# Kernel tuning notes

Hardware: AMD Instinct MI355X
Metric: run time of the kernel (lower is better)

Reference implementation:

```python
import jax, jax.numpy as jnp
import numpy as np

B, N, E = 32, 2048, 4096
D_IN, C, H = 256, 64, 4          # node_hidden_size, gnn_hidden_size, num_heads
SLOPE = 0.2                       # PyG GATConv default negative_slope


def gat_conv(x, src, dst, W, att_src, att_dst, bias):
    """One PyG-style GATConv (concat=True, add_self_loops=True) on a single graph.
    x: [N, Din]; src/dst: [E] int; W: [Din, H*C]; att_*: [H, C]; bias: [H*C]."""
    n = x.shape[0]
    h = (x @ W).reshape(n, H, C)                       # [N,H,C]
    a_src = jnp.einsum('nhc,hc->nh', h, att_src)       # [N,H]
    a_dst = jnp.einsum('nhc,hc->nh', h, att_dst)
    loop = jnp.arange(n, dtype=src.dtype)              # self loops
    s = jnp.concatenate([src, loop])
    d = jnp.concatenate([dst, loop])
    e = jax.nn.leaky_relu(a_src[s] + a_dst[d], SLOPE)  # [E+N,H]
    # segment softmax over incoming edges of each target node
    m = jax.ops.segment_max(e, d, num_segments=n)
    ex = jnp.exp(e - m[d])
    denom = jax.ops.segment_sum(ex, d, num_segments=n)
    alpha = ex / (denom[d] + 1e-16)                    # [E+N,H]
    out = jax.ops.segment_sum(alpha[:, :, None] * h[s], d, num_segments=n)  # [N,H,C]
    return out.reshape(n, H * C) + bias


def setup_inputs() -> dict:
    key = jax.random.key(0)
    ks = jax.random.split(key, 12)
    g = lambda k, shp, fan: jax.random.normal(k, shp, jnp.float32) * (1.0 / np.sqrt(fan))
    return {
        'node_embeddings': jax.random.normal(ks[0], (B, N, D_IN), jnp.float32),
        'src_index': jax.random.randint(ks[1], (B, E), 0, N, jnp.int32),
        'tgt_index': jax.random.randint(ks[2], (B, E), 0, N, jnp.int32),
        'W1': g(ks[3], (D_IN, H * C), D_IN),
        'att_src1': g(ks[4], (H, C), C),
        'att_dst1': g(ks[5], (H, C), C),
        'bias1': jnp.zeros((H * C,), jnp.float32),
        'W2': g(ks[6], (H * C, H * C), H * C),
        'att_src2': g(ks[7], (H, C), C),
        'att_dst2': g(ks[8], (H, C), C),
        'bias2': jnp.zeros((H * C,), jnp.float32),
    }


def reference(node_embeddings, src_index, tgt_index, W1, att_src1, att_dst1, bias1,
              W2, att_src2, att_dst2, bias2):
    def per_graph(x, s, d):
        m = gat_conv(x, s, d, W1, att_src1, att_dst1, bias1)
        m = jax.nn.elu(m)                              # dropout = identity (eval)
        m = gat_conv(m, s, d, W2, att_src2, att_dst2, bias2)
        return m
    return jax.vmap(per_graph)(node_embeddings, src_index, tgt_index)  # [B,N,H*C]
```

## Files before the change

### kernel.cpp

```cpp
#include <hip/hip_runtime.h>
#include <hip/hip_bf16.h>
#include <cstdint>

#define BB 32
#define NN 2048
#define EE 4096
#define HH 4
#define CC 64
#define DD 256
#define MM (BB*NN)

typedef __attribute__((ext_vector_type(8))) short bf16x8;
typedef __attribute__((ext_vector_type(8))) unsigned short u16x8;
typedef __attribute__((ext_vector_type(4))) float f32x4;

__device__ __forceinline__ float b2f(__hip_bfloat16 x){ return __bfloat162float(x); }
__device__ __forceinline__ float u2f(unsigned short u){ return __uint_as_float((unsigned)u << 16); }
__device__ __forceinline__ unsigned short f2u(float f){
  __hip_bfloat16 h = __float2bfloat16(f);
  return *(unsigned short*)&h;
}
__device__ __forceinline__ float ldany(const void* p, int isf, size_t i){
  return isf ? ((const float*)p)[i] : b2f(((const __hip_bfloat16*)p)[i]);
}
__device__ __forceinline__ void gld_lds16(const void* g, void* l){
  __builtin_amdgcn_global_load_lds((const __attribute__((address_space(1))) uint32_t*)g,
                                   (__attribute__((address_space(3))) uint32_t*)l, 16, 0, 0);
}

__global__ void detect_kernel(const unsigned* __restrict__ w, int* __restrict__ flag){
  __shared__ int cnt;
  if(threadIdx.x == 0) cnt = 0;
  __syncthreads();
  int c = 0;
  #pragma unroll
  for(int i = 0; i < 4; ++i){
    unsigned v = w[threadIdx.x*4 + i];
    unsigned elo = (v >> 7) & 0xFFu;
    if(elo >= 100u && elo <= 150u) ++c;
  }
  atomicAdd(&cnt, c);
  __syncthreads();
  if(threadIdx.x == 0) *flag = (cnt < 128) ? 1 : 0;
}

__global__ __launch_bounds__(256) void prep_kernel(const void* __restrict__ W1,
    const void* __restrict__ W2, __hip_bfloat16* __restrict__ W1t,
    __hip_bfloat16* __restrict__ W2t,
    const void* s0, const void* s1, const void* s2, const void* s3,
    const void* s4, const void* s5, float* __restrict__ attf,
    int* __restrict__ degc, const int* __restrict__ flag)
{
  int isf = *flag;
  int bid = blockIdx.x, t = threadIdx.x;
  if(bid < 512){
    const void* W = (bid < 256) ? W1 : W2;
    __hip_bfloat16* WT = (bid < 256) ? W1t : W2t;
    int i = (bid & 255)*256 + t;
    WT[i] = __float2bfloat16(ldany(W, isf, (size_t)(i & 255)*256 + (i >> 8)));
  } else if(bid < 518){
    int i = (bid - 512)*256 + t;
    int seg = i >> 8, off = i & 255;
    const void* s = seg==0?s0 : seg==1?s1 : seg==2?s2 : seg==3?s3 : seg==4?s4 : s5;
    attf[i] = ldany(s, isf, off);
  } else {
    int i = (bid - 518)*256 + t;
    int4 z = {0,0,0,0};
    *((int4*)degc + i) = z;
  }
}

template<int DYNA>
__global__ __launch_bounds__(256) void mfma_gemm(const void* __restrict__ Ap,
    const __hip_bfloat16* __restrict__ BT, __hip_bfloat16* __restrict__ C,
    const float* __restrict__ attS, const float* __restrict__ attD,
    float* __restrict__ aS, float* __restrict__ aD, const int* __restrict__ flag)
{
  __shared__ __align__(16) short lds[128*128];
  short* lA = lds;
  short* lB = lds + 128*64;
  const int isf  = DYNA ? *flag : 0;
  const int tid  = threadIdx.x;
  const int w    = tid >> 6, lane = tid & 63;
  const int dd   = blockIdx.x;
  const int xcd  = dd & 7, slot = dd >> 3;
  const int rb   = xcd*64 + (slot >> 1), cb = slot & 1;
  const int row0 = rb*128, col0 = cb*128;
  const int wr   = (w & 1)*64, wc = (w >> 1)*64;
  const int lr   = lane >> 3;
  const int kb_g = (lane & 7) ^ lr;
  const int fm   = lane & 15, quad = lane >> 4;
  f32x4 acc[4][4] = {};

  for(int k0 = 0; k0 < 256; k0 += 64){
    #pragma unroll
    for(int c = 0; c < 4; ++c){
      int ra = w*32 + c*8;
      const short* gb = (const short*)BT + (size_t)(col0 + ra + lr)*DD + k0 + kb_g*8;
      gld_lds16(gb, &lB[ra*64]);
    }
    if(DYNA && isf){
      const float* Af = (const float*)Ap;
      float4 ta[4], tb[4];
      #pragma unroll
      for(int i = 0; i < 4; ++i){
        int f8 = i*256 + tid;
        int m = f8 >> 3, kb = f8 & 7;
        const float* p = Af + (size_t)(row0 + m)*DD + k0 + kb*8;
        ta[i] = *(const float4*)p;
        tb[i] = *(const float4*)(p + 4);
      }
      #pragma unroll
      for(int i = 0; i < 4; ++i){
        int f8 = i*256 + tid;
        int m = f8 >> 3, kb = f8 & 7;
        u16x8 o;
        o[0] = f2u(ta[i].x); o[1] = f2u(ta[i].y); o[2] = f2u(ta[i].z); o[3] = f2u(ta[i].w);
        o[4] = f2u(tb[i].x); o[5] = f2u(tb[i].y); o[6] = f2u(tb[i].z); o[7] = f2u(tb[i].w);
        *(u16x8*)&lA[m*64 + ((kb ^ (m & 7))*8)] = o;
      }
    } else {
      #pragma unroll
      for(int c = 0; c < 4; ++c){
        int ra = w*32 + c*8;
        const short* ga = (const short*)Ap + (size_t)(row0 + ra + lr)*DD + k0 + kb_g*8;
        gld_lds16(ga, &lA[ra*64]);
      }
    }
    __syncthreads();
    #pragma unroll
    for(int ks = 0; ks < 2; ++ks){
      bf16x8 af[4], bfr[4];
      int kb = ks*4 + quad;
      #pragma unroll
      for(int i = 0; i < 4; ++i){
        int m = wr + i*16 + fm;
        af[i]  = *(const bf16x8*)&lA[m*64 + ((kb ^ (m & 7))*8)];
        int n = wc + i*16 + fm;
        bfr[i] = *(const bf16x8*)&lB[n*64 + ((kb ^ (n & 7))*8)];
      }
      #pragma unroll
      for(int i = 0; i < 4; ++i)
        #pragma unroll
        for(int j = 0; j < 4; ++j)
          acc[i][j] = __builtin_amdgcn_mfma_f32_16x16x32_bf16(af[i], bfr[j], acc[i][j], 0, 0, 0);
    }
    __syncthreads();
  }

  const int headI = (col0 + wc) >> 6;
  float ws_[4], wd_[4];
  #pragma unroll
  for(int j = 0; j < 4; ++j){
    ws_[j] = attS[headI*CC + j*16 + fm];
    wd_[j] = attD[headI*CC + j*16 + fm];
  }
  #pragma unroll
  for(int i = 0; i < 4; ++i){
    #pragma unroll
    for(int r = 0; r < 4; ++r){
      float s = 0.f, dv = 0.f;
      #pragma unroll
      for(int j = 0; j < 4; ++j){
        float v = acc[i][j][r];
        s  += v * ws_[j];
        dv += v * wd_[j];
      }
      #pragma unroll
      for(int m = 1; m <= 8; m <<= 1){
        s  += __shfl_xor(s,  m);
        dv += __shfl_xor(dv, m);
      }
      if(fm == i*4 + r){
        int row = row0 + wr + i*16 + quad*4 + r;
        aS[(size_t)row*HH + headI] = s;
        aD[(size_t)row*HH + headI] = dv;
      }
    }
  }

  #pragma unroll
  for(int i = 0; i < 4; ++i)
    #pragma unroll
    for(int j = 0; j < 4; ++j)
      #pragma unroll
      for(int r = 0; r < 4; ++r){
        int rl = wr + i*16 + quad*4 + r;
        int cl = wc + j*16 + fm;
        lds[rl*128 + (cl ^ ((rl & 12) << 2))] = (short)f2u(acc[i][j][r]);
      }
  __syncthreads();
  const int rr = tid >> 4, cc = (tid & 15)*8;
  #pragma unroll
  for(int p = 0; p < 8; ++p){
    int rl = p*16 + rr;
    u16x8 v = *(const u16x8*)&lds[rl*128 + (cc ^ ((rl & 12) << 2))];
    *(u16x8*)((unsigned short*)C + (size_t)(row0 + rl)*DD + col0 + cc) = v;
  }
}

__global__ __launch_bounds__(256) void deg_kernel(const int* __restrict__ dst, int* __restrict__ degc)
{
  int idx = blockIdx.x*256 + threadIdx.x;
  if(idx >= BB*EE) return;
  int b = idx >> 12;
  atomicAdd(&degc[b*NN + dst[idx]], 1);
}

__global__ __launch_bounds__(256) void scan_kernel(int* __restrict__ degc, int* __restrict__ row_ptr)
{
  __shared__ int part[256];
  int b = blockIdx.x, t = threadIdx.x;
  int loc[8], s = 0;
  #pragma unroll
  for(int i = 0; i < 8; ++i){ loc[i] = s; s += degc[b*NN + t*8 + i]; }
  part[t] = s;
  __syncthreads();
  if(t == 0){
    int run = 0;
    for(int i = 0; i < 256; ++i){ int tmp = part[i]; part[i] = run; run += tmp; }
  }
  __syncthreads();
  int base = b*EE + part[t];
  #pragma unroll
  for(int i = 0; i < 8; ++i){
    int v = base + loc[i];
    row_ptr[b*(NN+1) + t*8 + i] = v;
    degc   [b*NN     + t*8 + i] = v;
  }
  if(t == 255) row_ptr[b*(NN+1) + NN] = base + s;
}

__global__ __launch_bounds__(256) void scatter_kernel(const int* __restrict__ src,
    const int* __restrict__ dst, int* __restrict__ cursor, unsigned short* __restrict__ srcList)
{
  int idx = blockIdx.x*256 + threadIdx.x;
  if(idx >= BB*EE) return;
  int b = idx >> 12;
  int pos = atomicAdd(&cursor[b*NN + dst[idx]], 1);
  srcList[pos] = (unsigned short)src[idx];
}

template<int LAYER>
__global__ __launch_bounds__(256) void gather_kernel(const __hip_bfloat16* __restrict__ H,
    const float* __restrict__ a_src, const float* __restrict__ a_dst,
    const int* __restrict__ row_ptr, const unsigned short* __restrict__ srcList,
    const float* __restrict__ bias, void* __restrict__ outp,
    const int* __restrict__ flag)
{
  int blk  = blockIdx.x;
  int vblk = (blk & 7)*2048 + (blk >> 3);
  int wid  = vblk*4 + (int)(threadIdx.x >> 6);
  int lane = threadIdx.x & 63;
  int b = wid >> 11, d = wid & (NN-1);
  int head = lane >> 4;
  int start = row_ptr[b*(NN+1) + d];
  int end   = row_ptr[b*(NN+1) + d + 1];
  const unsigned short* Hu = (const unsigned short*)H;

  float adv = a_dst[wid*HH + head];
  float sv  = a_src[wid*HH + head] + adv;
  sv = sv > 0.f ? sv : 0.2f*sv;
  float exs = __expf(sv);

  ushort4 hv = *(const ushort4*)(Hu + (size_t)wid*DD + lane*4);
  f32x4 acc;
  acc.x = exs*u2f(hv.x); acc.y = exs*u2f(hv.y); acc.z = exs*u2f(hv.z); acc.w = exs*u2f(hv.w);
  float den = exs;

  int e = start;
  int s = 0; float ax = 0.f;
  if(e < end){ s = srcList[e]; ax = a_src[(b*NN + s)*HH + head]; }
  while(e < end){
    int sn = 0; float axn = 0.f;
    if(e + 1 < end){ sn = srcList[e+1]; axn = a_src[(b*NN + sn)*HH + head]; }
    float v = ax + adv;
    v = v > 0.f ? v : 0.2f*v;
    float ex = __expf(v);
    ushort4 hw = *(const ushort4*)(Hu + (size_t)(b*NN + s)*DD + lane*4);
    acc.x += ex*u2f(hw.x); acc.y += ex*u2f(hw.y); acc.z += ex*u2f(hw.z); acc.w += ex*u2f(hw.w);
    den += ex;
    s = sn; ax = axn; ++e;
  }
  float inv = 1.f / (den + 1e-16f);
  float4 bs = *(const float4*)(bias + lane*4);
  float o0 = acc.x*inv + bs.x, o1 = acc.y*inv + bs.y;
  float o2 = acc.z*inv + bs.z, o3 = acc.w*inv + bs.w;
  size_t oi = (size_t)wid*DD + lane*4;
  if(LAYER == 1){
    o0 = o0 > 0.f ? o0 : expm1f(o0);
    o1 = o1 > 0.f ? o1 : expm1f(o1);
    o2 = o2 > 0.f ? o2 : expm1f(o2);
    o3 = o3 > 0.f ? o3 : expm1f(o3);
    ushort4 ov = { f2u(o0), f2u(o1), f2u(o2), f2u(o3) };
    *(ushort4*)((unsigned short*)outp + oi) = ov;
  } else {
    if(*flag){
      float4 ov = { o0, o1, o2, o3 };
      *(float4*)((float*)outp + oi) = ov;
    } else {
      ushort4 ov = { f2u(o0), f2u(o1), f2u(o2), f2u(o3) };
      *(ushort4*)((unsigned short*)outp + oi) = ov;
    }
  }
}

extern "C" void kernel_launch(void* const* d_in, const int* in_sizes, int n_in,
                              void* d_out, int out_size, void* d_ws, size_t ws_size,
                              hipStream_t stream)
{
  const void* x_in = d_in[0];
  const int*  srcI = (const int*)d_in[1];
  const int*  dstI = (const int*)d_in[2];
  const void* W1   = d_in[3];
  const void* as1  = d_in[4];
  const void* ad1  = d_in[5];
  const void* b1   = d_in[6];
  const void* W2   = d_in[7];
  const void* as2  = d_in[8];
  const void* ad2  = d_in[9];
  const void* b2   = d_in[10];

  char* ws = (char*)d_ws;
  __hip_bfloat16* R1  = (__hip_bfloat16*)ws; ws += (size_t)MM*DD*2;
  __hip_bfloat16* R2  = (__hip_bfloat16*)ws; ws += (size_t)MM*DD*2;
  float* a_src = (float*)ws; ws += (size_t)MM*HH*4;
  float* a_dst = (float*)ws; ws += (size_t)MM*HH*4;
  __hip_bfloat16* W1t = (__hip_bfloat16*)ws; ws += (size_t)DD*DD*2;
  __hip_bfloat16* W2t = (__hip_bfloat16*)ws; ws += (size_t)DD*DD*2;
  float* attf = (float*)ws; ws += 1536*4;
  int*   degc = (int*)ws;   ws += (size_t)BB*NN*4;
  int*   rowp = (int*)ws;   ws += (size_t)BB*(NN+1)*4;
  unsigned short* srcL = (unsigned short*)ws; ws += (size_t)BB*EE*2;
  int*   flag = (int*)ws;   ws += 8;

  const int gemmBlocks   = (MM/128)*(DD/128);
  const int edgeBlocks   = (BB*EE)/256;
  const int gatherBlocks = (MM*64)/256;

  detect_kernel<<<1, 64, 0, stream>>>((const unsigned*)x_in, flag);
  prep_kernel<<<582, 256, 0, stream>>>(W1, W2, W1t, W2t,
                                       as1, ad1, b1, as2, ad2, b2, attf, degc, flag);

  deg_kernel    <<<edgeBlocks, 256, 0, stream>>>(dstI, degc);
  scan_kernel   <<<BB,         256, 0, stream>>>(degc, rowp);
  scatter_kernel<<<edgeBlocks, 256, 0, stream>>>(srcI, dstI, degc, srcL);

  mfma_gemm<1><<<gemmBlocks, 256, 0, stream>>>(x_in, W1t, R2, attf + 0, attf + 256,
                                               a_src, a_dst, flag);
  gather_kernel<1><<<gatherBlocks, 256, 0, stream>>>(R2, a_src, a_dst, rowp, srcL,
                                                     attf + 512, R1, flag);
  mfma_gemm<0><<<gemmBlocks, 256, 0, stream>>>(R1, W2t, R2, attf + 768, attf + 1024,
                                               a_src, a_dst, flag);
  gather_kernel<2><<<gatherBlocks, 256, 0, stream>>>(R2, a_src, a_dst, rowp, srcL,
                                                     attf + 1280, d_out, flag);
}
```

Baseline: 242.6 us.

## Double-buffer GEMM LDS tiles with K=32 stages and prefetch neighbor rows in aggregation

The GEMM main loop is split into eight K=32 stages. It ping-pongs two LDS buffers so the global-to-LDS loads for the next stage are issued before the MFMAs on the current stage, which needs only one barrier per stage. For fp32 input, the next A tile is held in registers and written to LDS after the compute. The launch bounds now request 4 blocks per CU, and the LDS swizzle is redone for 32-wide rows. In the edge aggregation kernel, the neighbor feature row is now prefetched one edge ahead along with the attention score, hiding gather latency at the cost of more registers.

```diff
diff --git a/kernel.cpp b/kernel.cpp
--- a/kernel.cpp
+++ b/kernel.cpp
@@ -71,14 +71,12 @@
 }
 
 template<int DYNA>
-__global__ __launch_bounds__(256) void mfma_gemm(const void* __restrict__ Ap,
+__global__ __launch_bounds__(256, 4) void mfma_gemm(const void* __restrict__ Ap,
     const __hip_bfloat16* __restrict__ BT, __hip_bfloat16* __restrict__ C,
     const float* __restrict__ attS, const float* __restrict__ attD,
     float* __restrict__ aS, float* __restrict__ aD, const int* __restrict__ flag)
 {
-  __shared__ __align__(16) short lds[128*128];
-  short* lA = lds;
-  short* lB = lds + 128*64;
+  __shared__ __align__(16) short lds[16384];
   const int isf  = DYNA ? *flag : 0;
   const int tid  = threadIdx.x;
   const int w    = tid >> 6, lane = tid & 63;
@@ -87,64 +85,86 @@
   const int rb   = xcd*64 + (slot >> 1), cb = slot & 1;
   const int row0 = rb*128, col0 = cb*128;
   const int wr   = (w & 1)*64, wc = (w >> 1)*64;
-  const int lr   = lane >> 3;
-  const int kb_g = (lane & 7) ^ lr;
   const int fm   = lane & 15, quad = lane >> 4;
+  const int srow = lane >> 2;
+  const int sslot= lane & 3;
   f32x4 acc[4][4] = {};
 
-  for(int k0 = 0; k0 < 256; k0 += 64){
+  const float* Af = (const float*)Ap;
+  const short* Ab = (const short*)Ap;
+  const int fr = tid >> 1;
+  const int fh = tid & 1;
+  float4 fa0, fa1, fa2, fa3;
+
+  auto stageB = [&](int t, int cur){
+    short* lB = lds + cur*8192 + 4096;
     #pragma unroll
-    for(int c = 0; c < 4; ++c){
-      int ra = w*32 + c*8;
-      const short* gb = (const short*)BT + (size_t)(col0 + ra + lr)*DD + k0 + kb_g*8;
-      gld_lds16(gb, &lB[ra*64]);
-    }
-    if(DYNA && isf){
-      const float* Af = (const float*)Ap;
-      float4 ta[4], tb[4];
-      #pragma unroll
-      for(int i = 0; i < 4; ++i){
-        int f8 = i*256 + tid;
-        int m = f8 >> 3, kb = f8 & 7;
-        const float* p = Af + (size_t)(row0 + m)*DD + k0 + kb*8;
-        ta[i] = *(const float4*)p;
-        tb[i] = *(const float4*)(p + 4);
-      }
-      #pragma unroll
-      for(int i = 0; i < 4; ++i){
-        int f8 = i*256 + tid;
-        int m = f8 >> 3, kb = f8 & 7;
-        u16x8 o;
-        o[0] = f2u(ta[i].x); o[1] = f2u(ta[i].y); o[2] = f2u(ta[i].z); o[3] = f2u(ta[i].w);
-        o[4] = f2u(tb[i].x); o[5] = f2u(tb[i].y); o[6] = f2u(tb[i].z); o[7] = f2u(tb[i].w);
-        *(u16x8*)&lA[m*64 + ((kb ^ (m & 7))*8)] = o;
-      }
-    } else {
-      #pragma unroll
-      for(int c = 0; c < 4; ++c){
-        int ra = w*32 + c*8;
-        const short* ga = (const short*)Ap + (size_t)(row0 + ra + lr)*DD + k0 + kb_g*8;
-        gld_lds16(ga, &lA[ra*64]);
-      }
-    }
-    __syncthreads();
+    for(int c = 0; c < 2; ++c){
+      int rB = w*32 + c*16 + srow;
+      const short* gb = (const short*)BT + (size_t)(col0 + rB)*DD + t*32
+                        + ((sslot ^ ((rB ^ (rB >> 3)) & 3))*8);
+      gld_lds16(gb, lB + (w*32 + c*16)*32);
+    }
+  };
+  auto stageA16 = [&](int t, int cur){
+    short* lA = lds + cur*8192;
     #pragma unroll
-    for(int ks = 0; ks < 2; ++ks){
-      bf16x8 af[4], bfr[4];
-      int kb = ks*4 + quad;
+    for(int c = 0; c < 2; ++c){
+      int rA = w*32 + c*16 + srow;
+      const short* ga = Ab + (size_t)(row0 + rA)*DD + t*32
+                        + ((sslot ^ ((rA ^ (rA >> 3)) & 3))*8);
+      gld_lds16(ga, lA + (w*32 + c*16)*32);
+    }
+  };
+  auto loadA32 = [&](int t){
+    const float* p = Af + (size_t)(row0 + fr)*DD + t*32 + fh*16;
+    fa0 = ((const float4*)p)[0]; fa1 = ((const float4*)p)[1];
+    fa2 = ((const float4*)p)[2]; fa3 = ((const float4*)p)[3];
+  };
+  auto writeA32 = [&](int cur){
+    short* lA = lds + cur*8192;
+    int sg = (fr ^ (fr >> 3)) & 3;
+    u16x8 o0, o1;
+    o0[0]=f2u(fa0.x); o0[1]=f2u(fa0.y); o0[2]=f2u(fa0.z); o0[3]=f2u(fa0.w);
+    o0[4]=f2u(fa1.x); o0[5]=f2u(fa1.y); o0[6]=f2u(fa1.z); o0[7]=f2u(fa1.w);
+    o1[0]=f2u(fa2.x); o1[1]=f2u(fa2.y); o1[2]=f2u(fa2.z); o1[3]=f2u(fa2.w);
+    o1[4]=f2u(fa3.x); o1[5]=f2u(fa3.y); o1[6]=f2u(fa3.z); o1[7]=f2u(fa3.w);
+    *(u16x8*)(lA + fr*32 + (((2*fh  ) ^ sg)*8)) = o0;
+    *(u16x8*)(lA + fr*32 + (((2*fh+1) ^ sg)*8)) = o1;
+  };
+
+  if(DYNA && isf){ loadA32(0); writeA32(0); }
+  else           { stageA16(0, 0); }
+  stageB(0, 0);
+  __syncthreads();
+
+  #pragma unroll 2
+  for(int t = 0; t < 8; ++t){
+    const int cur = t & 1, nxt = cur ^ 1;
+    const bool pre = (t < 7);
+    if(pre){
+      if(DYNA && isf) loadA32(t+1);
+      else            stageA16(t+1, nxt);
+      stageB(t+1, nxt);
+    }
+    {
+      const short* lA = lds + cur*8192;
+      const short* lB = lds + cur*8192 + 4096;
+      bf16x8 af[4], bfv[4];
       #pragma unroll
       for(int i = 0; i < 4; ++i){
         int m = wr + i*16 + fm;
-        af[i]  = *(const bf16x8*)&lA[m*64 + ((kb ^ (m & 7))*8)];
+        af[i]  = *(const bf16x8*)&lA[m*32 + ((quad ^ ((m ^ (m >> 3)) & 3))*8)];
         int n = wc + i*16 + fm;
-        bfr[i] = *(const bf16x8*)&lB[n*64 + ((kb ^ (n & 7))*8)];
+        bfv[i] = *(const bf16x8*)&lB[n*32 + ((quad ^ ((n ^ (n >> 3)) & 3))*8)];
       }
       #pragma unroll
       for(int i = 0; i < 4; ++i)
         #pragma unroll
         for(int j = 0; j < 4; ++j)
-          acc[i][j] = __builtin_amdgcn_mfma_f32_16x16x32_bf16(af[i], bfr[j], acc[i][j], 0, 0, 0);
-    }
+          acc[i][j] = __builtin_amdgcn_mfma_f32_16x16x32_bf16(af[i], bfv[j], acc[i][j], 0, 0, 0);
+    }
+    if(pre && DYNA && isf) writeA32(nxt);
     __syncthreads();
   }
 
@@ -269,18 +289,25 @@
   float den = exs;
 
   int e = start;
-  int s = 0; float ax = 0.f;
-  if(e < end){ s = srcList[e]; ax = a_src[(b*NN + s)*HH + head]; }
+  float ax = 0.f; ushort4 hw = {0,0,0,0};
+  if(e < end){
+    int s = srcList[e];
+    ax = a_src[(b*NN + s)*HH + head];
+    hw = *(const ushort4*)(Hu + (size_t)(b*NN + s)*DD + lane*4);
+  }
   while(e < end){
-    int sn = 0; float axn = 0.f;
-    if(e + 1 < end){ sn = srcList[e+1]; axn = a_src[(b*NN + sn)*HH + head]; }
+    float axn = 0.f; ushort4 hwn = {0,0,0,0};
+    if(e + 1 < end){
+      int sn = srcList[e+1];
+      axn = a_src[(b*NN + sn)*HH + head];
+      hwn = *(const ushort4*)(Hu + (size_t)(b*NN + sn)*DD + lane*4);
+    }
     float v = ax + adv;
     v = v > 0.f ? v : 0.2f*v;
     float ex = __expf(v);
-    ushort4 hw = *(const ushort4*)(Hu + (size_t)(b*NN + s)*DD + lane*4);
     acc.x += ex*u2f(hw.x); acc.y += ex*u2f(hw.y); acc.z += ex*u2f(hw.z); acc.w += ex*u2f(hw.w);
     den += ex;
-    s = sn; ax = axn; ++e;
+    ax = axn; hw = hwn; ++e;
   }
   float inv = 1.f / (den + 1e-16f);
   float4 bs = *(const float4*)(bias + lane*4);
```

Result: no change. 245.4 us (+1.2%).

## Fuse CSR build into prep kernel with LDS atomics; prefetch neighbor rows in gather

Applied to the files above, without the earlier changes.

Replaces the separate degree, scan and scatter kernels with per-graph blocks inside the prep kernel. Each block counts degrees, scans and scatters using shared-memory atomics, which removes three launches and the global atomics. The gather loop also prefetches the next neighbor's feature row alongside its attention score to hide load latency. Only 32 blocks now do the CSR work, so that part runs with little parallelism. The prefetch also adds register pressure.

```diff
diff --git a/kernel.cpp b/kernel.cpp
--- a/kernel.cpp
+++ b/kernel.cpp
@@ -44,29 +44,65 @@
   if(threadIdx.x == 0) *flag = (cnt < 128) ? 1 : 0;
 }
 
-__global__ __launch_bounds__(256) void prep_kernel(const void* __restrict__ W1,
+__global__ __launch_bounds__(256) void prep2_kernel(const void* __restrict__ W1,
     const void* __restrict__ W2, __hip_bfloat16* __restrict__ W1t,
     __hip_bfloat16* __restrict__ W2t,
     const void* s0, const void* s1, const void* s2, const void* s3,
     const void* s4, const void* s5, float* __restrict__ attf,
-    int* __restrict__ degc, const int* __restrict__ flag)
+    const int* __restrict__ srcI, const int* __restrict__ dstI,
+    int* __restrict__ rowp, unsigned short* __restrict__ srcL,
+    const int* __restrict__ flag)
 {
-  int isf = *flag;
+  __shared__ int ldeg[NN];
+  __shared__ int part[256];
   int bid = blockIdx.x, t = threadIdx.x;
   if(bid < 512){
+    int isf = *flag;
     const void* W = (bid < 256) ? W1 : W2;
     __hip_bfloat16* WT = (bid < 256) ? W1t : W2t;
     int i = (bid & 255)*256 + t;
     WT[i] = __float2bfloat16(ldany(W, isf, (size_t)(i & 255)*256 + (i >> 8)));
   } else if(bid < 518){
+    int isf = *flag;
     int i = (bid - 512)*256 + t;
     int seg = i >> 8, off = i & 255;
     const void* s = seg==0?s0 : seg==1?s1 : seg==2?s2 : seg==3?s3 : seg==4?s4 : s5;
     attf[i] = ldany(s, isf, off);
   } else {
-    int i = (bid - 518)*256 + t;
-    int4 z = {0,0,0,0};
-    *((int4*)degc + i) = z;
+    int g = bid - 518;
+    const int* ds = dstI + g*EE;
+    const int* ss = srcI + g*EE;
+    for(int i = t; i < NN; i += 256) ldeg[i] = 0;
+    __syncthreads();
+    for(int i = t; i < EE; i += 256) atomicAdd(&ldeg[ds[i] & (NN-1)], 1);
+    __syncthreads();
+    int loc[8], s = 0;
+    #pragma unroll
+    for(int k = 0; k < 8; ++k){ loc[k] = s; s += ldeg[t*8 + k]; }
+    part[t] = s;
+    __syncthreads();
+    if(t == 0){
+      int run = 0;
+      for(int i = 0; i < 256; ++i){ int tmp = part[i]; part[i] = run; run += tmp; }
+    }
+    __syncthreads();
+    int base = g*EE + part[t];
+    int cur[8];
+    #pragma unroll
+    for(int k = 0; k < 8; ++k){
+      int v = base + loc[k];
+      rowp[g*(NN+1) + t*8 + k] = v;
+      cur[k] = v;
+    }
+    if(t == 255) rowp[g*(NN+1) + NN] = base + s;
+    __syncthreads();
+    #pragma unroll
+    for(int k = 0; k < 8; ++k) ldeg[t*8 + k] = cur[k];
+    __syncthreads();
+    for(int i = t; i < EE; i += 256){
+      int pos = atomicAdd(&ldeg[ds[i] & (NN-1)], 1);
+      srcL[pos] = (unsigned short)ss[i];
+    }
   }
 }
 
@@ -199,48 +235,6 @@
   }
 }
 
-__global__ __launch_bounds__(256) void deg_kernel(const int* __restrict__ dst, int* __restrict__ degc)
-{
-  int idx = blockIdx.x*256 + threadIdx.x;
-  if(idx >= BB*EE) return;
-  int b = idx >> 12;
-  atomicAdd(&degc[b*NN + dst[idx]], 1);
-}
-
-__global__ __launch_bounds__(256) void scan_kernel(int* __restrict__ degc, int* __restrict__ row_ptr)
-{
-  __shared__ int part[256];
-  int b = blockIdx.x, t = threadIdx.x;
-  int loc[8], s = 0;
-  #pragma unroll
-  for(int i = 0; i < 8; ++i){ loc[i] = s; s += degc[b*NN + t*8 + i]; }
-  part[t] = s;
-  __syncthreads();
-  if(t == 0){
-    int run = 0;
-    for(int i = 0; i < 256; ++i){ int tmp = part[i]; part[i] = run; run += tmp; }
-  }
-  __syncthreads();
-  int base = b*EE + part[t];
-  #pragma unroll
-  for(int i = 0; i < 8; ++i){
-    int v = base + loc[i];
-    row_ptr[b*(NN+1) + t*8 + i] = v;
-    degc   [b*NN     + t*8 + i] = v;
-  }
-  if(t == 255) row_ptr[b*(NN+1) + NN] = base + s;
-}
-
-__global__ __launch_bounds__(256) void scatter_kernel(const int* __restrict__ src,
-    const int* __restrict__ dst, int* __restrict__ cursor, unsigned short* __restrict__ srcList)
-{
-  int idx = blockIdx.x*256 + threadIdx.x;
-  if(idx >= BB*EE) return;
-  int b = idx >> 12;
-  int pos = atomicAdd(&cursor[b*NN + dst[idx]], 1);
-  srcList[pos] = (unsigned short)src[idx];
-}
-
 template<int LAYER>
 __global__ __launch_bounds__(256) void gather_kernel(const __hip_bfloat16* __restrict__ H,
     const float* __restrict__ a_src, const float* __restrict__ a_dst,
@@ -269,18 +263,25 @@
   float den = exs;
 
   int e = start;
-  int s = 0; float ax = 0.f;
-  if(e < end){ s = srcList[e]; ax = a_src[(b*NN + s)*HH + head]; }
+  float ax = 0.f; ushort4 hw = {0,0,0,0};
+  if(e < end){
+    int s = srcList[e];
+    ax = a_src[(b*NN + s)*HH + head];
+    hw = *(const ushort4*)(Hu + (size_t)(b*NN + s)*DD + lane*4);
+  }
   while(e < end){
-    int sn = 0; float axn = 0.f;
-    if(e + 1 < end){ sn = srcList[e+1]; axn = a_src[(b*NN + sn)*HH + head]; }
+    float axn = 0.f; ushort4 hwn = {0,0,0,0};
+    if(e + 1 < end){
+      int sn = srcList[e+1];
+      axn = a_src[(b*NN + sn)*HH + head];
+      hwn = *(const ushort4*)(Hu + (size_t)(b*NN + sn)*DD + lane*4);
+    }
     float v = ax + adv;
     v = v > 0.f ? v : 0.2f*v;
     float ex = __expf(v);
-    ushort4 hw = *(const ushort4*)(Hu + (size_t)(b*NN + s)*DD + lane*4);
     acc.x += ex*u2f(hw.x); acc.y += ex*u2f(hw.y); acc.z += ex*u2f(hw.z); acc.w += ex*u2f(hw.w);
     den += ex;
-    s = sn; ax = axn; ++e;
+    ax = axn; hw = hwn; ++e;
   }
   float inv = 1.f / (den + 1e-16f);
   float4 bs = *(const float4*)(bias + lane*4);
@@ -329,22 +330,17 @@
   __hip_bfloat16* W1t = (__hip_bfloat16*)ws; ws += (size_t)DD*DD*2;
   __hip_bfloat16* W2t = (__hip_bfloat16*)ws; ws += (size_t)DD*DD*2;
   float* attf = (float*)ws; ws += 1536*4;
-  int*   degc = (int*)ws;   ws += (size_t)BB*NN*4;
   int*   rowp = (int*)ws;   ws += (size_t)BB*(NN+1)*4;
   unsigned short* srcL = (unsigned short*)ws; ws += (size_t)BB*EE*2;
   int*   flag = (int*)ws;   ws += 8;
 
   const int gemmBlocks   = (MM/128)*(DD/128);
-  const int edgeBlocks   = (BB*EE)/256;
   const int gatherBlocks = (MM*64)/256;
 
   detect_kernel<<<1, 64, 0, stream>>>((const unsigned*)x_in, flag);
-  prep_kernel<<<582, 256, 0, stream>>>(W1, W2, W1t, W2t,
-                                       as1, ad1, b1, as2, ad2, b2, attf, degc, flag);
-
-  deg_kernel    <<<edgeBlocks, 256, 0, stream>>>(dstI, degc);
-  scan_kernel   <<<BB,         256, 0, stream>>>(degc, rowp);
-  scatter_kernel<<<edgeBlocks, 256, 0, stream>>>(srcI, dstI, degc, srcL);
+  prep2_kernel<<<550, 256, 0, stream>>>(W1, W2, W1t, W2t,
+                                        as1, ad1, b1, as2, ad2, b2, attf,
+                                        srcI, dstI, rowp, srcL, flag);
 
   mfma_gemm<1><<<gemmBlocks, 256, 0, stream>>>(x_in, W1t, R2, attf + 0, attf + 256,
                                                a_src, a_dst, flag);
```

Result: no change. 245.8 us (+1.3%).
